# Performance work log

Hardware: AMD Instinct MI355X
Metric: run time of the kernel (lower is better)

The kernel has to match this reference:

```python
import jax, jax.numpy as jnp
import numpy as np

EPS = 1e-06

def _sobel_kernels():
    kx = jnp.array([[-1.0, 0.0, 1.0], [-2.0, 0.0, 2.0], [-1.0, 0.0, 1.0]], dtype=jnp.float32)
    ky = jnp.array([[-1.0, -2.0, -1.0], [0.0, 0.0, 0.0], [1.0, 2.0, 1.0]], dtype=jnp.float32)
    # depthwise: [out_ch=3, in_ch/groups=1, 3, 3]
    fx = jnp.broadcast_to(kx, (3, 1, 3, 3))
    fy = jnp.broadcast_to(ky, (3, 1, 3, 3))
    return fx, fy

def _dwconv(x, w):
    # x: [B,3,H,W], w: [3,1,3,3], groups=3, padding=1
    return jax.lax.conv_general_dilated(
        x, w, window_strides=(1, 1), padding=((1, 1), (1, 1)),
        dimension_numbers=('NCHW', 'OIHW', 'NCHW'), feature_group_count=3)

def _edge_mag(img, fx, fy):
    ex = _dwconv(img, fx)
    ey = _dwconv(img, fy)
    return jnp.sqrt(ex * ex + ey * ey + EPS)

def setup_inputs() -> dict:
    key = jax.random.key(0)
    k1, k2 = jax.random.split(key)
    img1 = jax.random.uniform(k1, (16, 3, 512, 512), dtype=jnp.float32)
    img2 = jax.random.uniform(k2, (16, 3, 512, 512), dtype=jnp.float32)
    return {"img1": img1, "img2": img2}

def reference(img1, img2):
    fx, fy = _sobel_kernels()
    mag1 = _edge_mag(img1, fx, fy)
    mag2 = _edge_mag(img2, fx, fy)
    return jnp.mean(jnp.abs(mag1 - mag2))
```

## Files before the change

kernel.cpp:

```cpp
#include <hip/hip_runtime.h>
#include <hip/hip_bf16.h>

#define IMG_H 512
#define IMG_W 512
#define NBLOCKS 768
#define TOTAL_ELEMS (48LL * 512 * 512)

__device__ __forceinline__ float fast_sqrtf(float x) {
    float r; asm("v_sqrt_f32 %0, %1" : "=v"(r) : "v"(x)); return r;
}

__device__ __forceinline__ void load8(const float* __restrict__ p, float v[8]) {
    const float4 x = *reinterpret_cast<const float4*>(p);
    const float4 y = *reinterpret_cast<const float4*>(p + 4);
    v[0] = x.x; v[1] = x.y; v[2] = x.z; v[3] = x.w;
    v[4] = y.x; v[5] = y.y; v[6] = y.z; v[7] = y.w;
}

__device__ __forceinline__ void lds_read8(const float* __restrict__ s, float v[8]) {
    const float4 x = *reinterpret_cast<const float4*>(s);
    const float4 y = *reinterpret_cast<const float4*>(s + 4);
    v[0] = x.x; v[1] = x.y; v[2] = x.z; v[3] = x.w;
    v[4] = y.x; v[5] = y.y; v[6] = y.z; v[7] = y.w;
}

__device__ __forceinline__ void sobel_mag_row(const float t[8], const float m[8], const float b[8],
                                              int lane, float mag[8]) {
    float cs[8], rd[8];
#pragma unroll
    for (int j = 0; j < 8; ++j) {
        cs[j] = (t[j] + b[j]) + 2.0f * m[j];
        rd[j] = b[j] - t[j];
    }
    float csL = __shfl_up(cs[7], 1), csR = __shfl_down(cs[0], 1);
    float rdL = __shfl_up(rd[7], 1), rdR = __shfl_down(rd[0], 1);
    if (lane == 0)  { csL = 0.0f; rdL = 0.0f; }
    if (lane == 63) { csR = 0.0f; rdR = 0.0f; }
#pragma unroll
    for (int j = 0; j < 8; ++j) {
        const float ex = ((j == 7) ? csR : cs[j + 1]) - ((j == 0) ? csL : cs[j - 1]);
        const float ey = ((j == 0) ? rdL : rd[j - 1]) + 2.0f * rd[j] + ((j == 7) ? rdR : rd[j + 1]);
        mag[j] = fast_sqrtf(fmaf(ex, ex, fmaf(ey, ey, 1e-6f)));
    }
}

__global__ __launch_bounds__(512) void edge_loss_kernel(const float* __restrict__ img1,
                                                        const float* __restrict__ img2,
                                                        float* __restrict__ slots) {
    const int t = threadIdx.x;
    const int lane = t & 63;
    const int w = t >> 6;
    const int bid = blockIdx.x;
    const int swz = (bid & 7) * 96 + (bid >> 3);
    const int plane = swz >> 4;
    const int blk = swz & 15;
    const int yb = blk << 5;
    const int y0 = yb + (w << 2);
    const int x0 = lane << 3;
    const size_t base = (size_t)plane * (IMG_H * IMG_W);
    const float* p1 = img1 + base + x0;
    const float* p2 = img2 + base + x0;

    __shared__ float sh[2][8][2][IMG_W];
    __shared__ float wave_sums[8];

    float a[4][8], b[4][8];
#pragma unroll
    for (int r = 0; r < 4; ++r) {
        load8(p1 + (size_t)(y0 + r) * IMG_W, a[r]);
        load8(p2 + (size_t)(y0 + r) * IMG_W, b[r]);
    }

    float ha[8], hb[8];
    bool hzero = false;
    if (w == 0) {
        hzero = (yb == 0);
        const int y = hzero ? 0 : yb - 1;
        load8(p1 + (size_t)y * IMG_W, ha);
        load8(p2 + (size_t)y * IMG_W, hb);
    } else if (w == 7) {
        hzero = (yb + 32 == IMG_H);
        const int y = hzero ? IMG_H - 1 : yb + 32;
        load8(p1 + (size_t)y * IMG_W, ha);
        load8(p2 + (size_t)y * IMG_W, hb);
    }
    if ((w == 0 || w == 7) && hzero) {
#pragma unroll
        for (int j = 0; j < 8; ++j) { ha[j] = 0.0f; hb[j] = 0.0f; }
    }

    *reinterpret_cast<float4*>(&sh[0][w][0][x0])     = make_float4(a[0][0], a[0][1], a[0][2], a[0][3]);
    *reinterpret_cast<float4*>(&sh[0][w][0][x0 + 4]) = make_float4(a[0][4], a[0][5], a[0][6], a[0][7]);
    *reinterpret_cast<float4*>(&sh[0][w][1][x0])     = make_float4(a[3][0], a[3][1], a[3][2], a[3][3]);
    *reinterpret_cast<float4*>(&sh[0][w][1][x0 + 4]) = make_float4(a[3][4], a[3][5], a[3][6], a[3][7]);
    *reinterpret_cast<float4*>(&sh[1][w][0][x0])     = make_float4(b[0][0], b[0][1], b[0][2], b[0][3]);
    *reinterpret_cast<float4*>(&sh[1][w][0][x0 + 4]) = make_float4(b[0][4], b[0][5], b[0][6], b[0][7]);
    *reinterpret_cast<float4*>(&sh[1][w][1][x0])     = make_float4(b[3][0], b[3][1], b[3][2], b[3][3]);
    *reinterpret_cast<float4*>(&sh[1][w][1][x0 + 4]) = make_float4(b[3][4], b[3][5], b[3][6], b[3][7]);
    __syncthreads();

    float ta[8], tb[8], ba[8], bb[8];
    if (w == 0) {
#pragma unroll
        for (int j = 0; j < 8; ++j) { ta[j] = ha[j]; tb[j] = hb[j]; }
    } else {
        lds_read8(&sh[0][w - 1][1][x0], ta);
        lds_read8(&sh[1][w - 1][1][x0], tb);
    }
    if (w == 7) {
#pragma unroll
        for (int j = 0; j < 8; ++j) { ba[j] = ha[j]; bb[j] = hb[j]; }
    } else {
        lds_read8(&sh[0][w + 1][0][x0], ba);
        lds_read8(&sh[1][w + 1][0][x0], bb);
    }

    float m1[4][8];
    sobel_mag_row(ta,   a[0], a[1], lane, m1[0]);
    sobel_mag_row(a[0], a[1], a[2], lane, m1[1]);
    sobel_mag_row(a[1], a[2], a[3], lane, m1[2]);
    sobel_mag_row(a[2], a[3], ba,   lane, m1[3]);

    float sum = 0.0f;
    {
        float m2[8];
        sobel_mag_row(tb,   b[0], b[1], lane, m2);
#pragma unroll
        for (int j = 0; j < 8; ++j) sum += fabsf(m1[0][j] - m2[j]);
        sobel_mag_row(b[0], b[1], b[2], lane, m2);
#pragma unroll
        for (int j = 0; j < 8; ++j) sum += fabsf(m1[1][j] - m2[j]);
        sobel_mag_row(b[1], b[2], b[3], lane, m2);
#pragma unroll
        for (int j = 0; j < 8; ++j) sum += fabsf(m1[2][j] - m2[j]);
        sobel_mag_row(b[2], b[3], bb,   lane, m2);
#pragma unroll
        for (int j = 0; j < 8; ++j) sum += fabsf(m1[3][j] - m2[j]);
    }

#pragma unroll
    for (int off = 32; off > 0; off >>= 1) sum += __shfl_down(sum, off);

    if (lane == 0) wave_sums[w] = sum;
    __syncthreads();
    if (t == 0) {
        float s = 0.0f;
#pragma unroll
        for (int i = 0; i < 8; ++i) s += wave_sums[i];
        slots[bid] = s;
    }
}

__global__ __launch_bounds__(256) void finalize_kernel(const float* __restrict__ slots,
                                                       float* __restrict__ out) {
    const int t = threadIdx.x;
    const int lane = t & 63;
    const int w = t >> 6;
    float s = 0.0f;
#pragma unroll
    for (int i = 0; i < NBLOCKS / 256; ++i) s += slots[t + i * 256];
#pragma unroll
    for (int off = 32; off > 0; off >>= 1) s += __shfl_down(s, off);
    __shared__ float ws[4];
    if (lane == 0) ws[w] = s;
    __syncthreads();
    if (t == 0) out[0] = ((ws[0] + ws[1]) + (ws[2] + ws[3])) * (1.0f / (float)TOTAL_ELEMS);
}

extern "C" void kernel_launch(void* const* d_in, const int* in_sizes, int n_in,
                              void* d_out, int out_size, void* d_ws, size_t ws_size,
                              hipStream_t stream) {
    const float* img1 = (const float*)d_in[0];
    const float* img2 = (const float*)d_in[1];
    float* out = (float*)d_out;
    float* slots = (float*)d_ws;

    edge_loss_kernel<<<dim3(NBLOCKS), 512, 0, stream>>>(img1, img2, slots);
    finalize_kernel<<<dim3(1), 256, 0, stream>>>(slots, out);
}
```

Baseline: 24.39 us.

## Process three consecutive row tiles per block with LDS halo reuse

Launches 256 blocks instead of 768, and each block loops over three consecutive 32-row tiles of a plane. When the previous tile was in the same plane, its last row is reused from LDS as the top halo, which saves one global row load per image. The block-swizzle mapping is dropped and the finalize kernel now reads a single slot per thread. In exchange, only 256 blocks run on a 256-CU part, which lowers parallelism and latency hiding, and the loop adds extra barriers per block.

```diff
diff --git a/kernel.cpp b/kernel.cpp
--- a/kernel.cpp
+++ b/kernel.cpp
@@ -3,7 +3,7 @@
 
 #define IMG_H 512
 #define IMG_W 512
-#define NBLOCKS 768
+#define NBLOCKS 256
 #define TOTAL_ELEMS (48LL * 512 * 512)
 
 __device__ __forceinline__ float fast_sqrtf(float x) {
@@ -51,91 +51,105 @@
     const int lane = t & 63;
     const int w = t >> 6;
     const int bid = blockIdx.x;
-    const int swz = (bid & 7) * 96 + (bid >> 3);
-    const int plane = swz >> 4;
-    const int blk = swz & 15;
-    const int yb = blk << 5;
-    const int y0 = yb + (w << 2);
     const int x0 = lane << 3;
-    const size_t base = (size_t)plane * (IMG_H * IMG_W);
-    const float* p1 = img1 + base + x0;
-    const float* p2 = img2 + base + x0;
 
     __shared__ float sh[2][8][2][IMG_W];
     __shared__ float wave_sums[8];
 
-    float a[4][8], b[4][8];
+    float sum = 0.0f;
+
 #pragma unroll
-    for (int r = 0; r < 4; ++r) {
-        load8(p1 + (size_t)(y0 + r) * IMG_W, a[r]);
-        load8(p2 + (size_t)(y0 + r) * IMG_W, b[r]);
-    }
+    for (int k = 0; k < 3; ++k) {
+        const int tile = bid * 3 + k;
+        const int plane = tile >> 4;
+        const int blk = tile & 15;
+        const int yb = blk << 5;
+        const int y0 = yb + (w << 2);
+        const size_t base = (size_t)plane * (IMG_H * IMG_W);
+        const float* p1 = img1 + base + x0;
+        const float* p2 = img2 + base + x0;
 
-    float ha[8], hb[8];
-    bool hzero = false;
-    if (w == 0) {
-        hzero = (yb == 0);
-        const int y = hzero ? 0 : yb - 1;
-        load8(p1 + (size_t)y * IMG_W, ha);
-        load8(p2 + (size_t)y * IMG_W, hb);
-    } else if (w == 7) {
-        hzero = (yb + 32 == IMG_H);
-        const int y = hzero ? IMG_H - 1 : yb + 32;
-        load8(p1 + (size_t)y * IMG_W, ha);
-        load8(p2 + (size_t)y * IMG_W, hb);
-    }
-    if ((w == 0 || w == 7) && hzero) {
+        float ha[8], hb[8];
+        bool fromLds = false;
+        if (k > 0 && w == 0 && blk != 0) {
+            lds_read8(&sh[0][7][1][x0], ha);
+            lds_read8(&sh[1][7][1][x0], hb);
+            fromLds = true;
+        }
+        __syncthreads();
+
+        float a[4][8], b[4][8];
 #pragma unroll
-        for (int j = 0; j < 8; ++j) { ha[j] = 0.0f; hb[j] = 0.0f; }
-    }
+        for (int r = 0; r < 4; ++r) {
+            load8(p1 + (size_t)(y0 + r) * IMG_W, a[r]);
+            load8(p2 + (size_t)(y0 + r) * IMG_W, b[r]);
+        }
 
-    *reinterpret_cast<float4*>(&sh[0][w][0][x0])     = make_float4(a[0][0], a[0][1], a[0][2], a[0][3]);
-    *reinterpret_cast<float4*>(&sh[0][w][0][x0 + 4]) = make_float4(a[0][4], a[0][5], a[0][6], a[0][7]);
-    *reinterpret_cast<float4*>(&sh[0][w][1][x0])     = make_float4(a[3][0], a[3][1], a[3][2], a[3][3]);
-    *reinterpret_cast<float4*>(&sh[0][w][1][x0 + 4]) = make_float4(a[3][4], a[3][5], a[3][6], a[3][7]);
-    *reinterpret_cast<float4*>(&sh[1][w][0][x0])     = make_float4(b[0][0], b[0][1], b[0][2], b[0][3]);
-    *reinterpret_cast<float4*>(&sh[1][w][0][x0 + 4]) = make_float4(b[0][4], b[0][5], b[0][6], b[0][7]);
-    *reinterpret_cast<float4*>(&sh[1][w][1][x0])     = make_float4(b[3][0], b[3][1], b[3][2], b[3][3]);
-    *reinterpret_cast<float4*>(&sh[1][w][1][x0 + 4]) = make_float4(b[3][4], b[3][5], b[3][6], b[3][7]);
-    __syncthreads();
+        if (w == 0 && !fromLds) {
+            if (blk == 0) {
+#pragma unroll
+                for (int j = 0; j < 8; ++j) { ha[j] = 0.0f; hb[j] = 0.0f; }
+            } else {
+                load8(p1 + (size_t)(yb - 1) * IMG_W, ha);
+                load8(p2 + (size_t)(yb - 1) * IMG_W, hb);
+            }
+        } else if (w == 7) {
+            if (blk == 15) {
+#pragma unroll
+                for (int j = 0; j < 8; ++j) { ha[j] = 0.0f; hb[j] = 0.0f; }
+            } else {
+                load8(p1 + (size_t)(yb + 32) * IMG_W, ha);
+                load8(p2 + (size_t)(yb + 32) * IMG_W, hb);
+            }
+        }
 
-    float ta[8], tb[8], ba[8], bb[8];
-    if (w == 0) {
+        *reinterpret_cast<float4*>(&sh[0][w][0][x0])     = make_float4(a[0][0], a[0][1], a[0][2], a[0][3]);
+        *reinterpret_cast<float4*>(&sh[0][w][0][x0 + 4]) = make_float4(a[0][4], a[0][5], a[0][6], a[0][7]);
+        *reinterpret_cast<float4*>(&sh[0][w][1][x0])     = make_float4(a[3][0], a[3][1], a[3][2], a[3][3]);
+        *reinterpret_cast<float4*>(&sh[0][w][1][x0 + 4]) = make_float4(a[3][4], a[3][5], a[3][6], a[3][7]);
+        *reinterpret_cast<float4*>(&sh[1][w][0][x0])     = make_float4(b[0][0], b[0][1], b[0][2], b[0][3]);
+        *reinterpret_cast<float4*>(&sh[1][w][0][x0 + 4]) = make_float4(b[0][4], b[0][5], b[0][6], b[0][7]);
+        *reinterpret_cast<float4*>(&sh[1][w][1][x0])     = make_float4(b[3][0], b[3][1], b[3][2], b[3][3]);
+        *reinterpret_cast<float4*>(&sh[1][w][1][x0 + 4]) = make_float4(b[3][4], b[3][5], b[3][6], b[3][7]);
+        __syncthreads();
+
+        float ta[8], tb[8], ba[8], bb[8];
+        if (w == 0) {
 #pragma unroll
-        for (int j = 0; j < 8; ++j) { ta[j] = ha[j]; tb[j] = hb[j]; }
-    } else {
-        lds_read8(&sh[0][w - 1][1][x0], ta);
-        lds_read8(&sh[1][w - 1][1][x0], tb);
-    }
-    if (w == 7) {
+            for (int j = 0; j < 8; ++j) { ta[j] = ha[j]; tb[j] = hb[j]; }
+        } else {
+            lds_read8(&sh[0][w - 1][1][x0], ta);
+            lds_read8(&sh[1][w - 1][1][x0], tb);
+        }
+        if (w == 7) {
 #pragma unroll
-        for (int j = 0; j < 8; ++j) { ba[j] = ha[j]; bb[j] = hb[j]; }
-    } else {
-        lds_read8(&sh[0][w + 1][0][x0], ba);
-        lds_read8(&sh[1][w + 1][0][x0], bb);
-    }
+            for (int j = 0; j < 8; ++j) { ba[j] = ha[j]; bb[j] = hb[j]; }
+        } else {
+            lds_read8(&sh[0][w + 1][0][x0], ba);
+            lds_read8(&sh[1][w + 1][0][x0], bb);
+        }
 
-    float m1[4][8];
-    sobel_mag_row(ta,   a[0], a[1], lane, m1[0]);
-    sobel_mag_row(a[0], a[1], a[2], lane, m1[1]);
-    sobel_mag_row(a[1], a[2], a[3], lane, m1[2]);
-    sobel_mag_row(a[2], a[3], ba,   lane, m1[3]);
+        float m1[4][8];
+        sobel_mag_row(ta,   a[0], a[1], lane, m1[0]);
+        sobel_mag_row(a[0], a[1], a[2], lane, m1[1]);
+        sobel_mag_row(a[1], a[2], a[3], lane, m1[2]);
+        sobel_mag_row(a[2], a[3], ba,   lane, m1[3]);
 
-    float sum = 0.0f;
-    {
-        float m2[8];
-        sobel_mag_row(tb,   b[0], b[1], lane, m2);
+        {
+            float m2[8];
+            sobel_mag_row(tb,   b[0], b[1], lane, m2);
 #pragma unroll
-        for (int j = 0; j < 8; ++j) sum += fabsf(m1[0][j] - m2[j]);
-        sobel_mag_row(b[0], b[1], b[2], lane, m2);
+            for (int j = 0; j < 8; ++j) sum += fabsf(m1[0][j] - m2[j]);
+            sobel_mag_row(b[0], b[1], b[2], lane, m2);
 #pragma unroll
-        for (int j = 0; j < 8; ++j) sum += fabsf(m1[1][j] - m2[j]);
-        sobel_mag_row(b[1], b[2], b[3], lane, m2);
+            for (int j = 0; j < 8; ++j) sum += fabsf(m1[1][j] - m2[j]);
+            sobel_mag_row(b[1], b[2], b[3], lane, m2);
 #pragma unroll
-        for (int j = 0; j < 8; ++j) sum += fabsf(m1[2][j] - m2[j]);
-        sobel_mag_row(b[2], b[3], bb,   lane, m2);
+            for (int j = 0; j < 8; ++j) sum += fabsf(m1[2][j] - m2[j]);
+            sobel_mag_row(b[2], b[3], bb,   lane, m2);
 #pragma unroll
-        for (int j = 0; j < 8; ++j) sum += fabsf(m1[3][j] - m2[j]);
+            for (int j = 0; j < 8; ++j) sum += fabsf(m1[3][j] - m2[j]);
+        }
     }
 
 #pragma unroll
@@ -156,9 +170,7 @@
     const int t = threadIdx.x;
     const int lane = t & 63;
     const int w = t >> 6;
-    float s = 0.0f;
-#pragma unroll
-    for (int i = 0; i < NBLOCKS / 256; ++i) s += slots[t + i * 256];
+    float s = slots[t];
 #pragma unroll
     for (int off = 32; off > 0; off >>= 1) s += __shfl_down(s, off);
     __shared__ float ws[4];
```

Result: slower. 29.05 us (+19.1%).
